# Kernel tuning notes

Hardware: AMD Instinct MI355X
Metric: run time of the kernel (lower is better)

## Reference

```python
import jax, jax.numpy as jnp
import numpy as np

N, C = 16384, 512

def setup_inputs() -> dict:
    key = jax.random.key(0)
    k1, k2 = jax.random.split(key)
    mean = jax.random.normal(k1, (N, C), dtype=jnp.float32)
    var = jax.random.uniform(k2, (N, C), dtype=jnp.float32)  # positive diagonal variances
    return {"mean": mean, "var": var, "num_samples": 400}

def reference(mean, var, num_samples):
    # Monte Carlo estimate of E[softmax(mean + eps)], eps ~ N(0, diag(var)).
    # lax.scan keeps memory flat (no [S, N, C] buffer), matching the torch loop.
    std = jnp.sqrt(var)
    keys = jax.random.split(jax.random.key(42), num_samples)

    def body(acc, k):
        eps = jax.random.normal(k, mean.shape, dtype=mean.dtype) * std
        return acc + jax.nn.softmax(mean + eps, axis=-1), None

    acc, _ = jax.lax.scan(body, jnp.zeros_like(mean), keys)
    return acc / num_samples
```

## Files before the change

### kernel.cpp

```cpp
#include <hip/hip_runtime.h>
#include <stdint.h>

#define NSAMP 400
#define NC 512

#if __has_builtin(__builtin_amdgcn_exp2f)
#define EXP2F(x) __builtin_amdgcn_exp2f(x)
#else
#define EXP2F(x) __expf((x) * 0.6931471805599453f)
#endif
#if __has_builtin(__builtin_amdgcn_logf)
#define LOG2F(x) __builtin_amdgcn_logf(x)
#else
#define LOG2F(x) (__logf(x) * 1.4426950408889634f)
#endif

static __device__ __forceinline__ uint32_t rotl32(uint32_t v, int n) {
  return (v << n) | (v >> (32 - n));
}

#define TFS(x0, x1, R) { x0 += x1; x1 = rotl32(x1, R); x1 ^= x0; }
static __device__ __forceinline__ void threefry2x32_full(
    uint32_t k0, uint32_t k1, uint32_t x0, uint32_t x1,
    uint32_t& o0, uint32_t& o1)
{
  const uint32_t ks2 = k0 ^ k1 ^ 0x1BD11BDAu;
  x0 += k0; x1 += k1;
  TFS(x0,x1,13) TFS(x0,x1,15) TFS(x0,x1,26) TFS(x0,x1, 6)
  x0 += k1; x1 += ks2 + 1u;
  TFS(x0,x1,17) TFS(x0,x1,29) TFS(x0,x1,16) TFS(x0,x1,24)
  x0 += ks2; x1 += k0 + 2u;
  TFS(x0,x1,13) TFS(x0,x1,15) TFS(x0,x1,26) TFS(x0,x1, 6)
  x0 += k0; x1 += k1 + 3u;
  TFS(x0,x1,17) TFS(x0,x1,29) TFS(x0,x1,16) TFS(x0,x1,24)
  x0 += k1; x1 += ks2 + 4u;
  TFS(x0,x1,13) TFS(x0,x1,15) TFS(x0,x1,26) TFS(x0,x1, 6)
  x0 += ks2; x1 += k0 + 5u;
  o0 = x0; o1 = x1;
}

#define R3OP(R)          { x0 += x1; x1 = rotl32(x1, R) ^ x0; }
#define INJR(ka, kb, R)  { x1 += kb; x0 = x0 + x1 + ka; x1 = rotl32(x1, R) ^ x0; }

static __device__ __forceinline__ uint32_t tf_bits_fused(
    uint32_t k0, uint32_t k1, uint32_t ks2,
    uint32_t I1, uint32_t I2, uint32_t I3, uint32_t I4, uint32_t I5,
    uint32_t cnt)
{
  uint32_t x1 = cnt + k1;
  uint32_t x0 = x1 + k0;
  x1 = rotl32(x1, 13) ^ x0;
  R3OP(15) R3OP(26) R3OP(6)
  INJR(k1,  I1, 17) R3OP(29) R3OP(16) R3OP(24)
  INJR(ks2, I2, 13) R3OP(15) R3OP(26) R3OP(6)
  INJR(k0,  I3, 17) R3OP(29) R3OP(16) R3OP(24)
  INJR(k1,  I4, 13) R3OP(15) R3OP(26) R3OP(6)
  x0 += ks2; x1 += I5;
  return x0 ^ x1;
}

static __device__ __forceinline__ void bits2uL(uint32_t bits, float& u, float& L) {
  float f = __uint_as_float(__builtin_amdgcn_alignbit(0x7Fu, bits, 9u)) - 1.0f;
  u = fmaf(f, 2.0f, -0.99999994f);
  L = LOG2F(fmaf(u, -u, 1.0f));
}

static __device__ __forceinline__ float softexp(float u, float L, float sd2, float m2) {
  float p;
  if (L > -7.2134752f) {
    float w = fmaf(L, -0.69314718f, -2.5f);
    p =              2.81022636e-08f;
    p = fmaf(p, w,   3.43273939e-07f);
    p = fmaf(p, w,  -3.5233877e-06f);
    p = fmaf(p, w,  -4.39150654e-06f);
    p = fmaf(p, w,   0.00021858087f);
    p = fmaf(p, w,  -0.00125372503f);
    p = fmaf(p, w,  -0.00417768164f);
    p = fmaf(p, w,   0.246640727f);
    p = fmaf(p, w,   1.50140941f);
  } else {
    float w = __builtin_amdgcn_sqrtf(L * -0.69314718f) - 3.0f;
    p =             -0.000200214257f;
    p = fmaf(p, w,   0.000100950558f);
    p = fmaf(p, w,   0.00134934322f);
    p = fmaf(p, w,  -0.00367342844f);
    p = fmaf(p, w,   0.00573950773f);
    p = fmaf(p, w,  -0.0076224613f);
    p = fmaf(p, w,   0.00943887047f);
    p = fmaf(p, w,   1.00167406f);
    p = fmaf(p, w,   2.83297682f);
  }
  float px = p * u;
  return EXP2F(fmaf(px, sd2, m2));
}

static __device__ __forceinline__ uint32_t rfl(uint32_t x) {
  return (uint32_t)__builtin_amdgcn_readfirstlane((int)x);
}

template <int CTRL>
static __device__ __forceinline__ float dppadd(float x) {
  return x + __int_as_float(
      __builtin_amdgcn_update_dpp(0, __float_as_int(x), CTRL, 0xf, 0xf, false));
}
static __device__ __forceinline__ float wave_sum_bcast(float x) {
  x = dppadd<0x111>(x);
  x = dppadd<0x112>(x);
  x = dppadd<0x114>(x);
  x = dppadd<0x118>(x);
  x = dppadd<0x142>(x);
  x = dppadd<0x143>(x);
  return __uint_as_float((uint32_t)__builtin_amdgcn_readlane(__float_as_int(x), 63));
}

__global__ __launch_bounds__(256)
void mc_softmax_kernel(const float* __restrict__ mean,
                       const float* __restrict__ var,
                       float* __restrict__ out)
{
  __shared__ __align__(16) uint32_t kc[NSAMP][8];
  for (int s = threadIdx.x; s < NSAMP; s += 256) {
    uint32_t a, b;
    threefry2x32_full(0u, 42u, 0u, (uint32_t)s, a, b);
    uint32_t ks2 = a ^ b ^ 0x1BD11BDAu;
    kc[s][0] = a;        kc[s][1] = b;
    kc[s][2] = ks2;      kc[s][3] = ks2 + 1u;
    kc[s][4] = a + 2u;   kc[s][5] = b + 3u;
    kc[s][6] = ks2 + 4u; kc[s][7] = a + 5u;
  }
  __syncthreads();

  const int lane  = threadIdx.x & 63;
  const int row   = (blockIdx.x << 2) + (threadIdx.x >> 6);
  const int cbase = lane << 2;

  const float* mr = mean + (size_t)row * NC;
  const float* vr = var  + (size_t)row * NC;

  float m2[8], sd2[8], acc[8];
  {
    const float L2E = 1.4426950408889634f;
    const float S2L = 2.0402788959f;
    float4 t0 = *(const float4*)(mr + cbase);
    float4 t1 = *(const float4*)(mr + 256 + cbase);
    m2[0] = t0.x * L2E; m2[1] = t0.y * L2E; m2[2] = t0.z * L2E; m2[3] = t0.w * L2E;
    m2[4] = t1.x * L2E; m2[5] = t1.y * L2E; m2[6] = t1.z * L2E; m2[7] = t1.w * L2E;
    float4 v0 = *(const float4*)(vr + cbase);
    float4 v1 = *(const float4*)(vr + 256 + cbase);
    sd2[0] = __builtin_amdgcn_sqrtf(v0.x) * S2L;
    sd2[1] = __builtin_amdgcn_sqrtf(v0.y) * S2L;
    sd2[2] = __builtin_amdgcn_sqrtf(v0.z) * S2L;
    sd2[3] = __builtin_amdgcn_sqrtf(v0.w) * S2L;
    sd2[4] = __builtin_amdgcn_sqrtf(v1.x) * S2L;
    sd2[5] = __builtin_amdgcn_sqrtf(v1.y) * S2L;
    sd2[6] = __builtin_amdgcn_sqrtf(v1.z) * S2L;
    sd2[7] = __builtin_amdgcn_sqrtf(v1.w) * S2L;
  }
#pragma unroll
  for (int j = 0; j < 8; ++j) acc[j] = 0.0f;

  const uint32_t base = (uint32_t)(row * NC + cbase);
  uint32_t cnt[8];
#pragma unroll
  for (int j = 0; j < 4; ++j) { cnt[j] = base + (uint32_t)j; cnt[4+j] = base + 256u + (uint32_t)j; }

  for (int s = 0; s < NSAMP; s += 2) {
    const uint4 a0 = *(const uint4*)&kc[s][0];
    const uint4 a1 = *(const uint4*)&kc[s][4];
    const uint4 b0 = *(const uint4*)&kc[s + 1][0];
    const uint4 b1 = *(const uint4*)&kc[s + 1][4];
    const uint32_t Ak0 = rfl(a0.x), Ak1 = rfl(a0.y), Aks = rfl(a0.z), AI1 = rfl(a0.w);
    const uint32_t AI2 = rfl(a1.x), AI3 = rfl(a1.y), AI4 = rfl(a1.z), AI5 = rfl(a1.w);
    const uint32_t Bk0 = rfl(b0.x), Bk1 = rfl(b0.y), Bks = rfl(b0.z), BI1 = rfl(b0.w);
    const uint32_t BI2 = rfl(b1.x), BI3 = rfl(b1.y), BI4 = rfl(b1.z), BI5 = rfl(b1.w);

    float uA[8], LA[8];
#pragma unroll
    for (int j = 0; j < 8; ++j) {
      uint32_t bits = tf_bits_fused(Ak0, Ak1, Aks, AI1, AI2, AI3, AI4, AI5, cnt[j]);
      bits2uL(bits, uA[j], LA[j]);
    }
    float eA[8], sA = 0.0f;
#pragma unroll
    for (int j = 0; j < 8; ++j) { eA[j] = softexp(uA[j], LA[j], sd2[j], m2[j]); sA += eA[j]; }

    float uB[8], LB[8];
#pragma unroll
    for (int j = 0; j < 8; ++j) {
      uint32_t bits = tf_bits_fused(Bk0, Bk1, Bks, BI1, BI2, BI3, BI4, BI5, cnt[j]);
      bits2uL(bits, uB[j], LB[j]);
    }

    const float invA = __builtin_amdgcn_rcpf(wave_sum_bcast(sA));
#pragma unroll
    for (int j = 0; j < 8; ++j) acc[j] = fmaf(eA[j], invA, acc[j]);

    float eB[8], sB = 0.0f;
#pragma unroll
    for (int j = 0; j < 8; ++j) { eB[j] = softexp(uB[j], LB[j], sd2[j], m2[j]); sB += eB[j]; }

    const float invB = __builtin_amdgcn_rcpf(wave_sum_bcast(sB));
#pragma unroll
    for (int j = 0; j < 8; ++j) acc[j] = fmaf(eB[j], invB, acc[j]);
  }

  float* orow = out + (size_t)row * NC;
  const float sc = 1.0f / (float)NSAMP;
  float4 o0, o1;
  o0.x = acc[0] * sc; o0.y = acc[1] * sc; o0.z = acc[2] * sc; o0.w = acc[3] * sc;
  o1.x = acc[4] * sc; o1.y = acc[5] * sc; o1.z = acc[6] * sc; o1.w = acc[7] * sc;
  *(float4*)(orow + cbase)       = o0;
  *(float4*)(orow + 256 + cbase) = o1;
}

extern "C" void kernel_launch(void* const* d_in, const int* in_sizes, int n_in,
                              void* d_out, int out_size, void* d_ws, size_t ws_size,
                              hipStream_t stream) {
  const float* mean = (const float*)d_in[0];
  const float* var  = (const float*)d_in[1];
  float* out        = (float*)d_out;

  const int rows = out_size / NC;
  const int blocks = rows / 4;
  mc_softmax_kernel<<<blocks, 256, 0, stream>>>(mean, var, out);
}
```

Baseline: 6.575 ms.

## Micro-optimize Threefry ops, prefetch sample keys, and tree-reduce softmax sums

Rotations now use alignbit, and key injection uses an inline-asm v_add3_u32 that takes an SGPR operand. The per-sample key constants are loaded from LDS one iteration ahead to hide LDS latency. The common branch of the inverse-erf polynomial is hinted as likely, and the per-thread exp sums become a pairwise tree instead of a serial chain. These are several small ALU and latency tweaks, and the inline asm may limit the compiler's scheduling.

```diff
diff --git a/kernel.cpp b/kernel.cpp
--- a/kernel.cpp
+++ b/kernel.cpp
@@ -16,7 +16,13 @@
 #endif
 
 static __device__ __forceinline__ uint32_t rotl32(uint32_t v, int n) {
-  return (v << n) | (v >> (32 - n));
+  return __builtin_amdgcn_alignbit(v, v, (uint32_t)(32 - n));
+}
+
+static __device__ __forceinline__ uint32_t add3s(uint32_t a, uint32_t b, uint32_t c) {
+  uint32_t d;
+  asm("v_add3_u32 %0, %1, %2, %3" : "=v"(d) : "v"(a), "v"(b), "s"(c));
+  return d;
 }
 
 #define TFS(x0, x1, R) { x0 += x1; x1 = rotl32(x1, R); x1 ^= x0; }
@@ -40,7 +46,7 @@
 }
 
 #define R3OP(R)          { x0 += x1; x1 = rotl32(x1, R) ^ x0; }
-#define INJR(ka, kb, R)  { x1 += kb; x0 = x0 + x1 + ka; x1 = rotl32(x1, R) ^ x0; }
+#define INJR(ka, kb, R)  { x1 += kb; x0 = add3s(x0, x1, ka); x1 = rotl32(x1, R) ^ x0; }
 
 static __device__ __forceinline__ uint32_t tf_bits_fused(
     uint32_t k0, uint32_t k1, uint32_t ks2,
@@ -67,7 +73,7 @@
 
 static __device__ __forceinline__ float softexp(float u, float L, float sd2, float m2) {
   float p;
-  if (L > -7.2134752f) {
+  if (__builtin_expect(L > -7.2134752f, 1)) {
     float w = fmaf(L, -0.69314718f, -2.5f);
     p =              2.81022636e-08f;
     p = fmaf(p, w,   3.43273939e-07f);
@@ -164,15 +170,22 @@
 #pragma unroll
   for (int j = 0; j < 4; ++j) { cnt[j] = base + (uint32_t)j; cnt[4+j] = base + 256u + (uint32_t)j; }
 
+  uint4 pa0 = *(const uint4*)&kc[0][0];
+  uint4 pa1 = *(const uint4*)&kc[0][4];
+  uint4 pb0 = *(const uint4*)&kc[1][0];
+  uint4 pb1 = *(const uint4*)&kc[1][4];
+
   for (int s = 0; s < NSAMP; s += 2) {
-    const uint4 a0 = *(const uint4*)&kc[s][0];
-    const uint4 a1 = *(const uint4*)&kc[s][4];
-    const uint4 b0 = *(const uint4*)&kc[s + 1][0];
-    const uint4 b1 = *(const uint4*)&kc[s + 1][4];
-    const uint32_t Ak0 = rfl(a0.x), Ak1 = rfl(a0.y), Aks = rfl(a0.z), AI1 = rfl(a0.w);
-    const uint32_t AI2 = rfl(a1.x), AI3 = rfl(a1.y), AI4 = rfl(a1.z), AI5 = rfl(a1.w);
-    const uint32_t Bk0 = rfl(b0.x), Bk1 = rfl(b0.y), Bks = rfl(b0.z), BI1 = rfl(b0.w);
-    const uint32_t BI2 = rfl(b1.x), BI3 = rfl(b1.y), BI4 = rfl(b1.z), BI5 = rfl(b1.w);
+    const uint32_t Ak0 = rfl(pa0.x), Ak1 = rfl(pa0.y), Aks = rfl(pa0.z), AI1 = rfl(pa0.w);
+    const uint32_t AI2 = rfl(pa1.x), AI3 = rfl(pa1.y), AI4 = rfl(pa1.z), AI5 = rfl(pa1.w);
+    const uint32_t Bk0 = rfl(pb0.x), Bk1 = rfl(pb0.y), Bks = rfl(pb0.z), BI1 = rfl(pb0.w);
+    const uint32_t BI2 = rfl(pb1.x), BI3 = rfl(pb1.y), BI4 = rfl(pb1.z), BI5 = rfl(pb1.w);
+
+    const int sn = (s + 2 < NSAMP) ? s + 2 : 0;
+    pa0 = *(const uint4*)&kc[sn][0];
+    pa1 = *(const uint4*)&kc[sn][4];
+    pb0 = *(const uint4*)&kc[sn + 1][0];
+    pb1 = *(const uint4*)&kc[sn + 1][4];
 
     float uA[8], LA[8];
 #pragma unroll
@@ -180,9 +193,11 @@
       uint32_t bits = tf_bits_fused(Ak0, Ak1, Aks, AI1, AI2, AI3, AI4, AI5, cnt[j]);
       bits2uL(bits, uA[j], LA[j]);
     }
-    float eA[8], sA = 0.0f;
-#pragma unroll
-    for (int j = 0; j < 8; ++j) { eA[j] = softexp(uA[j], LA[j], sd2[j], m2[j]); sA += eA[j]; }
+    float eA[8];
+#pragma unroll
+    for (int j = 0; j < 8; ++j) eA[j] = softexp(uA[j], LA[j], sd2[j], m2[j]);
+    const float sA = ((eA[0] + eA[1]) + (eA[2] + eA[3]))
+                   + ((eA[4] + eA[5]) + (eA[6] + eA[7]));
 
     float uB[8], LB[8];
 #pragma unroll
@@ -195,9 +210,11 @@
 #pragma unroll
     for (int j = 0; j < 8; ++j) acc[j] = fmaf(eA[j], invA, acc[j]);
 
-    float eB[8], sB = 0.0f;
-#pragma unroll
-    for (int j = 0; j < 8; ++j) { eB[j] = softexp(uB[j], LB[j], sd2[j], m2[j]); sB += eB[j]; }
+    float eB[8];
+#pragma unroll
+    for (int j = 0; j < 8; ++j) eB[j] = softexp(uB[j], LB[j], sd2[j], m2[j]);
+    const float sB = ((eB[0] + eB[1]) + (eB[2] + eB[3]))
+                   + ((eB[4] + eB[5]) + (eB[6] + eB[7]));
 
     const float invB = __builtin_amdgcn_rcpf(wave_sum_bcast(sB));
 #pragma unroll
```

Measured after the change: 6.665 ms. Within noise of the previous version (+1.4%).
